# Optimization experiments

Measured on AMD Instinct MI355X. Metric: run time of the kernel, lower is better.

Reference implementation:

```python
import jax, jax.numpy as jnp
import numpy as np

N, E = 50000, 800000
H, KC, EC, NH = 64, 64, 32, 4   # hidden, key, edge channels, heads
HPH, KPH = H // NH, KC // NH    # per-head value/key dims (16, 16)


def ssp(x):
    # ShiftedSoftplus
    return jax.nn.softplus(x) - jnp.log(2.0).astype(x.dtype)


def grouped_lin(x, w):
    # x: (N, NH, in_per_head), w: (NH, out_per_head, in_per_head)
    # equivalent to Conv1d(kernel=1, groups=NH, bias=False)
    return jnp.einsum('nhi,hoi->nho', x, w)


def lin(x, w, b):
    return x @ w.T + b


def segment_softmax(logits, seg, num_segments):
    # logits: (E, NH), seg: (E,)
    m = jax.ops.segment_max(logits, seg, num_segments=num_segments)
    m = jnp.where(jnp.isfinite(m), m, 0.0)
    e = jnp.exp(logits - m[seg])
    s = jax.ops.segment_sum(e, seg, num_segments=num_segments)
    return e / s[seg]


def setup_inputs() -> dict:
    key = jax.random.key(0)
    ks = jax.random.split(key, 24)
    sc = 0.05
    inp = {
        'x': jax.random.normal(ks[0], (N, H), jnp.float32),
        'edge_index': jax.random.randint(ks[1], (2, E), 0, N, jnp.int64),
        'edge_attr': jax.random.normal(ks[2], (E, EC), jnp.float32),
        # grouped 1x1 convs (block-diagonal linears), no bias
        'k_w': jax.random.normal(ks[3], (NH, KPH, HPH), jnp.float32) * sc,
        'q_w': jax.random.normal(ks[4], (NH, KPH, HPH), jnp.float32) * sc,
        'v_w': jax.random.normal(ks[5], (NH, HPH, HPH), jnp.float32) * sc,
        # weight_k_net: Linear(EC,KPH) -> ssp -> Linear(KPH,KPH)
        'wkn_w1': jax.random.normal(ks[6], (KPH, EC), jnp.float32) * sc,
        'wkn_b1': jnp.zeros((KPH,), jnp.float32),
        'wkn_w2': jax.random.normal(ks[7], (KPH, KPH), jnp.float32) * sc,
        'wkn_b2': jnp.zeros((KPH,), jnp.float32),
        'wkl_w': jax.random.normal(ks[8], (KPH, KPH), jnp.float32) * sc,
        'wkl_b': jnp.zeros((KPH,), jnp.float32),
        # weight_v_net: Linear(EC,HPH) -> ssp -> Linear(HPH,HPH)
        'wvn_w1': jax.random.normal(ks[9], (HPH, EC), jnp.float32) * sc,
        'wvn_b1': jnp.zeros((HPH,), jnp.float32),
        'wvn_w2': jax.random.normal(ks[10], (HPH, HPH), jnp.float32) * sc,
        'wvn_b2': jnp.zeros((HPH,), jnp.float32),
        'wvl_w': jax.random.normal(ks[11], (HPH, HPH), jnp.float32) * sc,
        'wvl_b': jnp.zeros((HPH,), jnp.float32),
        'cen_w': jax.random.normal(ks[12], (H, H), jnp.float32) * sc,
        'cen_b': jnp.zeros((H,), jnp.float32),
        'out_w': jax.random.normal(ks[13], (H, H), jnp.float32) * sc,
        'out_b': jnp.zeros((H,), jnp.float32),
    }
    return inp


def reference(x, edge_index, edge_attr, k_w, q_w, v_w,
              wkn_w1, wkn_b1, wkn_w2, wkn_b2, wkl_w, wkl_b,
              wvn_w1, wvn_b1, wvn_w2, wvn_b2, wvl_w, wvl_b,
              cen_w, cen_b, out_w, out_b):
    n = x.shape[0]
    row, col = edge_index[0], edge_index[1]
    xh = x.reshape(n, NH, HPH)                       # per-head split of channels
    h_keys = grouped_lin(xh, k_w)                    # (N, NH, KPH)
    h_queries = grouped_lin(xh, q_w)                 # (N, NH, KPH)
    h_values = grouped_lin(xh, v_w)                  # (N, NH, HPH)

    W_k = lin(ssp(lin(edge_attr, wkn_w1, wkn_b1)), wkn_w2, wkn_b2)   # (E, KPH)
    keys_j = lin(W_k[:, None, :] * h_keys[col], wkl_w, wkl_b)        # (E, NH, KPH)
    queries_i = h_queries[row]                                       # (E, NH, KPH)
    qk_ij = jnp.sum(queries_i * keys_j, axis=-1)                     # (E, NH)
    alpha = segment_softmax(qk_ij, row, n)                           # (E, NH)

    W_v = lin(ssp(lin(edge_attr, wvn_w1, wvn_b1)), wvn_w2, wvn_b2)   # (E, HPH)
    msg_j = lin(W_v[:, None, :] * h_values[col], wvl_w, wvl_b)       # (E, NH, HPH)
    msg_j = alpha[:, :, None] * msg_j
    aggr = jax.ops.segment_sum(msg_j, row, num_segments=n).reshape(n, H)

    out = lin(x, cen_w, cen_b) + aggr
    return lin(ssp(out), out_w, out_b)
```

## Files before the change

kernel.cpp:

```cpp
#include <hip/hip_runtime.h>
#include <math.h>
#include <stdint.h>

#define NN 50000
#define NE 800000
#define HD 64
#define ECH 32
#define NHEAD 4
#define NBLK 196

static_assert(NE % 256 == 0, "edge kernel assumes full blocks");

typedef __attribute__((ext_vector_type(8))) short bf8;
typedef __attribute__((ext_vector_type(4))) float f32x4;

__device__ __forceinline__ float ssp_f(float v) {
    return fmaxf(v, 0.0f) + log1pf(__expf(-fabsf(v))) - 0.69314718055994531f;
}
__device__ __forceinline__ uint32_t f2bf_bits(float f) {
    uint32_t u = __float_as_uint(f);
    return (u + 0x7FFFu + ((u >> 16) & 1u)) >> 16;
}
__device__ __forceinline__ float bf2f(uint32_t b) { return __uint_as_float(b << 16); }

__device__ __forceinline__ void unpack8(uint4 p, float* o) {
    o[0] = bf2f(p.x & 0xffffu); o[1] = bf2f(p.x >> 16);
    o[2] = bf2f(p.y & 0xffffu); o[3] = bf2f(p.y >> 16);
    o[4] = bf2f(p.z & 0xffffu); o[5] = bf2f(p.z >> 16);
    o[6] = bf2f(p.w & 0xffffu); o[7] = bf2f(p.w >> 16);
}
__device__ __forceinline__ uint4 pack8u(const float* s) {
    uint4 r;
    r.x = f2bf_bits(s[0]) | (f2bf_bits(s[1]) << 16);
    r.y = f2bf_bits(s[2]) | (f2bf_bits(s[3]) << 16);
    r.z = f2bf_bits(s[4]) | (f2bf_bits(s[5]) << 16);
    r.w = f2bf_bits(s[6]) | (f2bf_bits(s[7]) << 16);
    return r;
}
__device__ __forceinline__ bf8 pack_bf8(float4 a, float4 b) {
    bf8 r;
    r[0] = (short)f2bf_bits(a.x); r[1] = (short)f2bf_bits(a.y);
    r[2] = (short)f2bf_bits(a.z); r[3] = (short)f2bf_bits(a.w);
    r[4] = (short)f2bf_bits(b.x); r[5] = (short)f2bf_bits(b.y);
    r[6] = (short)f2bf_bits(b.z); r[7] = (short)f2bf_bits(b.w);
    return r;
}
__device__ __forceinline__ bf8 zero_bf8() {
    bf8 r;
    #pragma unroll
    for (int i = 0; i < 8; ++i) r[i] = 0;
    return r;
}

__global__ __launch_bounds__(256) void node_transform_kernel(
    const float* __restrict__ x,
    const float* __restrict__ k_w, const float* __restrict__ q_w, const float* __restrict__ v_w,
    const float* __restrict__ wkl_w, const float* __restrict__ wkl_b,
    uint16_t* __restrict__ qt, float* __restrict__ qb,
    uint16_t* __restrict__ hk, uint16_t* __restrict__ hv)
{
    __shared__ float skw[NHEAD * 256], sqw[NHEAD * 256], svw[NHEAD * 256];
    __shared__ float s_kl[256], s_klb[16];
    for (int i = threadIdx.x; i < NHEAD * 256; i += 256) {
        skw[i] = k_w[i]; sqw[i] = q_w[i]; svw[i] = v_w[i];
    }
    if (threadIdx.x < 256) s_kl[threadIdx.x] = wkl_w[threadIdx.x];
    if (threadIdx.x < 16) s_klb[threadIdx.x] = wkl_b[threadIdx.x];
    __syncthreads();
    int n = blockIdx.x * 256 + threadIdx.x;
    if (n >= NN) return;
    const float* xn = x + (size_t)n * HD;
    float qbv[NHEAD];
    for (int h = 0; h < NHEAD; ++h) {
        float xr[16];
        {
            const float4* xp = (const float4*)(xn + h * 16);
            #pragma unroll
            for (int j = 0; j < 4; ++j) *(float4*)&xr[4 * j] = xp[j];
        }
        float rq[16], rk[16], rv[16];
        for (int o = 0; o < 16; ++o) {
            const float* wq = sqw + h * 256 + o * 16;
            const float* wk = skw + h * 256 + o * 16;
            const float* wv = svw + h * 256 + o * 16;
            float sq = 0.f, sk = 0.f, sv = 0.f;
            #pragma unroll
            for (int i = 0; i < 16; ++i) {
                sq += xr[i] * wq[i];
                sk += xr[i] * wk[i];
                sv += xr[i] * wv[i];
            }
            rq[o] = sq; rk[o] = sk; rv[o] = sv;
        }
        float rqt[16];
        float qbh = 0.f;
        for (int i = 0; i < 16; ++i) {
            float s = 0.f;
            #pragma unroll
            for (int o = 0; o < 16; ++o) s += rq[o] * s_kl[o * 16 + i];
            rqt[i] = s;
        }
        #pragma unroll
        for (int o = 0; o < 16; ++o) qbh += rq[o] * s_klb[o];
        qbv[h] = qbh;

        uint4* oq = (uint4*)(qt + (size_t)n * HD + h * 16);
        uint4* ok = (uint4*)(hk + (size_t)n * HD + h * 16);
        uint4* ov = (uint4*)(hv + (size_t)n * HD + h * 16);
        oq[0] = pack8u(rqt); oq[1] = pack8u(rqt + 8);
        ok[0] = pack8u(rk);  ok[1] = pack8u(rk + 8);
        ov[0] = pack8u(rv);  ov[1] = pack8u(rv + 8);
    }
    *(float4*)(qb + (size_t)n * NHEAD) = *(float4*)&qbv[0];
}

__global__ __launch_bounds__(256) void count_kernel(
    const int* __restrict__ ei, int* __restrict__ counts)
{
    int e = blockIdx.x * 256 + threadIdx.x;
    if (e >= NE) return;
    atomicAdd(counts + ei[e], 1);
}

__global__ __launch_bounds__(256) void scan_bsum_kernel(
    const int* __restrict__ counts, int* __restrict__ bsum)
{
    __shared__ int sd[256];
    int i = blockIdx.x * 256 + threadIdx.x;
    sd[threadIdx.x] = (i < NN) ? counts[i] : 0;
    __syncthreads();
    for (int s = 128; s > 0; s >>= 1) {
        if (threadIdx.x < (unsigned)s) sd[threadIdx.x] += sd[threadIdx.x + s];
        __syncthreads();
    }
    if (threadIdx.x == 0) bsum[blockIdx.x] = sd[0];
}

__global__ __launch_bounds__(256) void scan_top_kernel(int* __restrict__ bsum)
{
    __shared__ int tmp[256];
    int v = (threadIdx.x < NBLK) ? bsum[threadIdx.x] : 0;
    tmp[threadIdx.x] = v;
    __syncthreads();
    for (int d = 1; d < 256; d <<= 1) {
        int t = (threadIdx.x >= (unsigned)d) ? tmp[threadIdx.x - d] : 0;
        __syncthreads();
        tmp[threadIdx.x] += t;
        __syncthreads();
    }
    if (threadIdx.x < NBLK) bsum[threadIdx.x] = tmp[threadIdx.x] - v;
}

__global__ __launch_bounds__(256) void scan_final_kernel(
    const int* __restrict__ counts, const int* __restrict__ bsum,
    int* __restrict__ offsets, int* __restrict__ cursor)
{
    __shared__ int tmp[256];
    int i = blockIdx.x * 256 + threadIdx.x;
    int v = (i < NN) ? counts[i] : 0;
    tmp[threadIdx.x] = v;
    __syncthreads();
    for (int d = 1; d < 256; d <<= 1) {
        int t = (threadIdx.x >= (unsigned)d) ? tmp[threadIdx.x - d] : 0;
        __syncthreads();
        tmp[threadIdx.x] += t;
        __syncthreads();
    }
    int excl = tmp[threadIdx.x] - v + bsum[blockIdx.x];
    if (i < NN) { offsets[i] = excl; cursor[i] = excl; }
}

__global__ __launch_bounds__(256) void scatter_kernel(
    const int* __restrict__ ei, int* __restrict__ cursor,
    int* __restrict__ elist, int2* __restrict__ rc)
{
    int e = blockIdx.x * 256 + threadIdx.x;
    if (e >= NE) return;
    int r = ei[e];
    int c = ei[NE + e];
    int pos = atomicAdd(cursor + r, 1);
    elist[pos] = e;
    rc[pos] = make_int2(r, c);
}

__global__ __launch_bounds__(256) void edge_compute_kernel(
    const int* __restrict__ elist, const int2* __restrict__ rc,
    const float* __restrict__ ea,
    const float* __restrict__ wkn_w1, const float* __restrict__ wkn_b1,
    const float* __restrict__ wkn_w2, const float* __restrict__ wkn_b2,
    const float* __restrict__ wvn_w1, const float* __restrict__ wvn_b1,
    const float* __restrict__ wvn_w2, const float* __restrict__ wvn_b2,
    const uint16_t* __restrict__ qt, const float* __restrict__ qb,
    const uint16_t* __restrict__ hk, const uint16_t* __restrict__ hv,
    uint16_t* __restrict__ payload, float* __restrict__ wfac)
{
    __shared__ uint16_t s_tr1[4][64][24];
    __shared__ uint16_t s_trk[4][64][24];
    __shared__ uint16_t s_trv[4][64][24];

    const int w = threadIdx.x >> 6;
    const int L = threadIdx.x & 63;
    const int m = L & 15;
    const int g = L >> 4;
    const int ebase = blockIdx.x * 256 + w * 64;

    int2 rcv[4];
    #pragma unroll
    for (int t = 0; t < 4; ++t) rcv[t] = rc[ebase + 16 * t + m];

    bf8 eaf[4];
    #pragma unroll
    for (int t = 0; t < 4; ++t) {
        int eid = elist[ebase + 16 * t + m];
        const float* er = ea + (size_t)eid * ECH + 8 * g;
        eaf[t] = pack_bf8(*(const float4*)er, *(const float4*)(er + 4));
    }
    bf8 w1kf, w1vf, w2kf, w2vf;
    {
        const float* p = wkn_w1 + m * 32 + 8 * g;
        w1kf = pack_bf8(*(const float4*)p, *(const float4*)(p + 4));
        p = wvn_w1 + m * 32 + 8 * g;
        w1vf = pack_bf8(*(const float4*)p, *(const float4*)(p + 4));
        if (g < 2) {
            p = wkn_w2 + m * 16 + 8 * g;
            w2kf = pack_bf8(*(const float4*)p, *(const float4*)(p + 4));
            p = wvn_w2 + m * 16 + 8 * g;
            w2vf = pack_bf8(*(const float4*)p, *(const float4*)(p + 4));
        } else {
            w2kf = zero_bf8(); w2vf = zero_bf8();
        }
    }
    float4 b1k = *(const float4*)(wkn_b1 + 4 * g);
    float4 b1v = *(const float4*)(wvn_b1 + 4 * g);
    float4 b2k = *(const float4*)(wkn_b2 + 4 * g);
    float4 b2v = *(const float4*)(wvn_b2 + 4 * g);

    #pragma unroll
    for (int t = 0; t < 4; ++t) {
        f32x4 acc = {b1k.x, b1k.y, b1k.z, b1k.w};
        acc = __builtin_amdgcn_mfma_f32_16x16x32_bf16(w1kf, eaf[t], acc, 0, 0, 0);
        uint2 pk;
        pk.x = f2bf_bits(ssp_f(acc[0])) | (f2bf_bits(ssp_f(acc[1])) << 16);
        pk.y = f2bf_bits(ssp_f(acc[2])) | (f2bf_bits(ssp_f(acc[3])) << 16);
        *(uint2*)&s_tr1[w][16 * t + m][4 * g] = pk;
    }
    bf8 l1k[4];
    #pragma unroll
    for (int t = 0; t < 4; ++t)
        l1k[t] = (g < 2) ? *(const bf8*)&s_tr1[w][16 * t + m][8 * g] : zero_bf8();
    #pragma unroll
    for (int t = 0; t < 4; ++t) {
        f32x4 acc = {b1v.x, b1v.y, b1v.z, b1v.w};
        acc = __builtin_amdgcn_mfma_f32_16x16x32_bf16(w1vf, eaf[t], acc, 0, 0, 0);
        uint2 pk;
        pk.x = f2bf_bits(ssp_f(acc[0])) | (f2bf_bits(ssp_f(acc[1])) << 16);
        pk.y = f2bf_bits(ssp_f(acc[2])) | (f2bf_bits(ssp_f(acc[3])) << 16);
        *(uint2*)&s_tr1[w][16 * t + m][4 * g] = pk;
    }
    bf8 l1v[4];
    #pragma unroll
    for (int t = 0; t < 4; ++t)
        l1v[t] = (g < 2) ? *(const bf8*)&s_tr1[w][16 * t + m][8 * g] : zero_bf8();

    #pragma unroll
    for (int t = 0; t < 4; ++t) {
        f32x4 acc = {b2k.x, b2k.y, b2k.z, b2k.w};
        acc = __builtin_amdgcn_mfma_f32_16x16x32_bf16(w2kf, l1k[t], acc, 0, 0, 0);
        uint2 pk;
        pk.x = f2bf_bits(acc[0]) | (f2bf_bits(acc[1]) << 16);
        pk.y = f2bf_bits(acc[2]) | (f2bf_bits(acc[3]) << 16);
        *(uint2*)&s_trk[w][16 * t + m][4 * g] = pk;

        f32x4 accv = {b2v.x, b2v.y, b2v.z, b2v.w};
        accv = __builtin_amdgcn_mfma_f32_16x16x32_bf16(w2vf, l1v[t], accv, 0, 0, 0);
        uint2 pv;
        pv.x = f2bf_bits(accv[0]) | (f2bf_bits(accv[1]) << 16);
        pv.y = f2bf_bits(accv[2]) | (f2bf_bits(accv[3]) << 16);
        *(uint2*)&s_trv[w][16 * t + m][4 * g] = pv;
    }

    #pragma unroll
    for (int t = 0; t < 4; ++t) {
        const int E = ebase + 16 * t + m;
        const int row = rcv[t].x, col = rcv[t].y;

        float Wk[16], Wv[16];
        unpack8(*(const uint4*)&s_trk[w][16 * t + m][0], Wk);
        unpack8(*(const uint4*)&s_trk[w][16 * t + m][8], Wk + 8);
        unpack8(*(const uint4*)&s_trv[w][16 * t + m][0], Wv);
        unpack8(*(const uint4*)&s_trv[w][16 * t + m][8], Wv + 8);

        const uint4* qp = (const uint4*)(qt + (size_t)row * HD + 16 * g);
        const uint4* kp = (const uint4*)(hk + (size_t)col * HD + 16 * g);
        const uint4* vp = (const uint4*)(hv + (size_t)col * HD + 16 * g);
        float qr[16], kc[16], vc[16];
        unpack8(qp[0], qr); unpack8(qp[1], qr + 8);
        unpack8(kp[0], kc); unpack8(kp[1], kc + 8);
        unpack8(vp[0], vc); unpack8(vp[1], vc + 8);

        float qk = qb[(size_t)row * NHEAD + g];
        #pragma unroll
        for (int i = 0; i < 16; ++i) qk += qr[i] * Wk[i] * kc[i];
        float wgt = __expf(qk);

        float o[16];
        #pragma unroll
        for (int i = 0; i < 16; ++i) o[i] = wgt * Wv[i] * vc[i];
        uint4* pd = (uint4*)(payload + (size_t)E * HD + 16 * g);
        pd[0] = pack8u(o);
        pd[1] = pack8u(o + 8);
        wfac[(size_t)E * NHEAD + g] = wgt;
    }
}

__global__ __launch_bounds__(256) void gather_finalize_kernel(
    const float* __restrict__ x,
    const uint16_t* __restrict__ payload, const float* __restrict__ wfac,
    const int* __restrict__ offsets, const int* __restrict__ counts,
    const float* __restrict__ wvl_w, const float* __restrict__ wvl_b,
    const float* __restrict__ cen_w, const float* __restrict__ cen_b,
    const float* __restrict__ out_w, const float* __restrict__ out_b,
    float* __restrict__ out)
{
    __shared__ float s_cw[4096], s_ow[4096];
    __shared__ float s_wvl[256], s_vlb[16];
    __shared__ float s_m[4][64], s_x[4][64], s_t[4][64];
    for (int idx = threadIdx.x; idx < 4096; idx += 256) {
        int o = idx & 63, i = idx >> 6;
        s_cw[i * 64 + o] = cen_w[o * 64 + i];
        s_ow[i * 64 + o] = out_w[o * 64 + i];
    }
    if (threadIdx.x < 256) s_wvl[threadIdx.x] = wvl_w[threadIdx.x];
    if (threadIdx.x < 16) s_vlb[threadIdx.x] = wvl_b[threadIdx.x];
    __syncthreads();

    int l = threadIdx.x >> 6;
    int L = threadIdx.x & 63;
    int q = L & 7;
    int g = L >> 3;
    int h = q >> 1;

    for (int t = 0; t < 16; ++t) {
        int n = blockIdx.x * 64 + l * 16 + t;
        bool valid = n < NN;
        int st = 0, deg = 0;
        if (valid) { st = offsets[n]; deg = counts[n]; }
        float u[8] = {0.f, 0.f, 0.f, 0.f, 0.f, 0.f, 0.f, 0.f};
        float ds = 0.f;
        const uint16_t* pp = payload + (size_t)st * HD + 8 * q;
        const float* wp = wfac + (size_t)st * NHEAD + h;
        int iters = (deg + 7) >> 3;
        for (int i = 0; i < iters; ++i) {
            int e = 8 * i + g;
            if (e < deg) {
                uint4 pv = *(const uint4*)(pp + (size_t)e * HD);
                u[0] += bf2f(pv.x & 0xffffu); u[1] += bf2f(pv.x >> 16);
                u[2] += bf2f(pv.y & 0xffffu); u[3] += bf2f(pv.y >> 16);
                u[4] += bf2f(pv.z & 0xffffu); u[5] += bf2f(pv.z >> 16);
                u[6] += bf2f(pv.w & 0xffffu); u[7] += bf2f(pv.w >> 16);
                ds += wp[(size_t)e * NHEAD];
            }
        }
        #pragma unroll
        for (int s = 8; s < 64; s <<= 1) {
            #pragma unroll
            for (int j = 0; j < 8; ++j) u[j] += __shfl_xor(u[j], s);
            ds += __shfl_xor(ds, s);
        }
        if (g == 0) {
            float inv = (deg > 0) ? (1.f / ds) : 0.f;
            float r0[4] = {u[0] * inv, u[1] * inv, u[2] * inv, u[3] * inv};
            float r1[4] = {u[4] * inv, u[5] * inv, u[6] * inv, u[7] * inv};
            *(float4*)&s_m[l][8 * q] = *(float4*)r0;
            *(float4*)&s_m[l][8 * q + 4] = *(float4*)r1;
        }
        s_x[l][L] = valid ? x[(size_t)n * HD + L] : 0.f;

        int c = L, hh = c >> 4;
        float aggr = 0.f;
        if (deg > 0) {
            int o = c & 15;
            float s = s_vlb[o];
            #pragma unroll
            for (int i = 0; i < 16; ++i) s += s_m[l][hh * 16 + i] * s_wvl[o * 16 + i];
            aggr = s;
        }
        float sc = cen_b[c];
        #pragma unroll 8
        for (int i = 0; i < 64; ++i) sc += s_x[l][i] * s_cw[i * 64 + c];
        sc += aggr;
        s_t[l][c] = ssp_f(sc);
        float so = out_b[c];
        #pragma unroll 8
        for (int i = 0; i < 64; ++i) so += s_t[l][i] * s_ow[i * 64 + c];
        if (valid) out[(size_t)n * HD + c] = so;
    }
}

extern "C" void kernel_launch(void* const* d_in, const int* in_sizes, int n_in,
                              void* d_out, int out_size, void* d_ws, size_t ws_size,
                              hipStream_t stream)
{
    const float* x      = (const float*)d_in[0];
    const int*   ei     = (const int*)d_in[1];
    const float* ea     = (const float*)d_in[2];
    const float* k_w    = (const float*)d_in[3];
    const float* q_w    = (const float*)d_in[4];
    const float* v_w    = (const float*)d_in[5];
    const float* wkn_w1 = (const float*)d_in[6];
    const float* wkn_b1 = (const float*)d_in[7];
    const float* wkn_w2 = (const float*)d_in[8];
    const float* wkn_b2 = (const float*)d_in[9];
    const float* wkl_w  = (const float*)d_in[10];
    const float* wkl_b  = (const float*)d_in[11];
    const float* wvn_w1 = (const float*)d_in[12];
    const float* wvn_b1 = (const float*)d_in[13];
    const float* wvn_w2 = (const float*)d_in[14];
    const float* wvn_b2 = (const float*)d_in[15];
    const float* wvl_w  = (const float*)d_in[16];
    const float* wvl_b  = (const float*)d_in[17];
    const float* cen_w  = (const float*)d_in[18];
    const float* cen_b  = (const float*)d_in[19];
    const float* out_w  = (const float*)d_in[20];
    const float* out_b  = (const float*)d_in[21];
    float* out = (float*)d_out;

    float* qb    = (float*)d_ws;
    float* wfac  = qb + (size_t)NN * NHEAD;
    uint16_t* qt = (uint16_t*)(wfac + (size_t)NE * NHEAD);
    uint16_t* hk = qt + (size_t)NN * HD;
    uint16_t* hv = hk + (size_t)NN * HD;
    uint16_t* payload = hv + (size_t)NN * HD;
    int2* rc     = (int2*)(payload + (size_t)NE * HD);
    int* elist   = (int*)(rc + (size_t)NE);
    int* counts  = elist + NE;
    int* bsum    = counts + NN;
    int* offsets = bsum + 256;
    int* cursor  = offsets + NN;

    hipMemsetAsync(counts, 0, (size_t)NN * sizeof(int), stream);
    node_transform_kernel<<<NBLK, 256, 0, stream>>>(
        x, k_w, q_w, v_w, wkl_w, wkl_b, qt, qb, hk, hv);
    count_kernel<<<(NE + 255) / 256, 256, 0, stream>>>(ei, counts);
    scan_bsum_kernel<<<NBLK, 256, 0, stream>>>(counts, bsum);
    scan_top_kernel<<<1, 256, 0, stream>>>(bsum);
    scan_final_kernel<<<NBLK, 256, 0, stream>>>(counts, bsum, offsets, cursor);
    scatter_kernel<<<(NE + 255) / 256, 256, 0, stream>>>(ei, cursor, elist, rc);
    edge_compute_kernel<<<NE / 256, 256, 0, stream>>>(
        elist, rc, ea, wkn_w1, wkn_b1, wkn_w2, wkn_b2,
        wvn_w1, wvn_b1, wvn_w2, wvn_b2,
        qt, qb, hk, hv, payload, wfac);
    gather_finalize_kernel<<<(NN + 63) / 64, 256, 0, stream>>>(
        x, payload, wfac, offsets, counts,
        wvl_w, wvl_b, cen_w, cen_b, out_w, out_b, out);
}
```

Measured before the change: 516.7 us.

## Fuse per-edge aggregation into edge kernel via LDS atomics, drop payload buffer

The edge kernel now accumulates weighted messages and softmax denominators per destination row. It uses shared-memory atomics over a window of up to CAP rows, then flushes to global numer/denom, using atomics only at the block-boundary rows or when the window overflows. This replaces the bf16 per-edge payload and the separate gather pass. The scatter kernel also writes edge attributes pre-sorted and converted to bf16, so the edge kernel no longer does an indirect fp32 read. The cost is a larger memset, LDS atomic contention, float atomic nondeterminism, and the unnormalized exp with no max subtraction that the base code already used.

```diff
diff --git a/kernel.cpp b/kernel.cpp
--- a/kernel.cpp
+++ b/kernel.cpp
@@ -8,6 +8,7 @@
 #define ECH 32
 #define NHEAD 4
 #define NBLK 196
+#define CAP 80
 
 static_assert(NE % 256 == 0, "edge kernel assumes full blocks");
 
@@ -153,7 +154,7 @@
 
 __global__ __launch_bounds__(256) void scan_final_kernel(
     const int* __restrict__ counts, const int* __restrict__ bsum,
-    int* __restrict__ offsets, int* __restrict__ cursor)
+    int* __restrict__ cursor)
 {
     __shared__ int tmp[256];
     int i = blockIdx.x * 256 + threadIdx.x;
@@ -167,42 +168,60 @@
         __syncthreads();
     }
     int excl = tmp[threadIdx.x] - v + bsum[blockIdx.x];
-    if (i < NN) { offsets[i] = excl; cursor[i] = excl; }
+    if (i < NN) cursor[i] = excl;
 }
 
 __global__ __launch_bounds__(256) void scatter_kernel(
-    const int* __restrict__ ei, int* __restrict__ cursor,
-    int* __restrict__ elist, int2* __restrict__ rc)
+    const int* __restrict__ ei, const float* __restrict__ ea,
+    int* __restrict__ cursor,
+    int2* __restrict__ rc, uint16_t* __restrict__ eaS)
 {
     int e = blockIdx.x * 256 + threadIdx.x;
     if (e >= NE) return;
     int r = ei[e];
     int c = ei[NE + e];
+    float eav[32];
+    const float4* p = (const float4*)(ea + (size_t)e * ECH);
+    #pragma unroll
+    for (int i = 0; i < 8; ++i) *(float4*)&eav[4 * i] = p[i];
     int pos = atomicAdd(cursor + r, 1);
-    elist[pos] = e;
     rc[pos] = make_int2(r, c);
-}
-
-__global__ __launch_bounds__(256) void edge_compute_kernel(
-    const int* __restrict__ elist, const int2* __restrict__ rc,
-    const float* __restrict__ ea,
+    uint4* d = (uint4*)(eaS + (size_t)pos * ECH);
+    d[0] = pack8u(eav);      d[1] = pack8u(eav + 8);
+    d[2] = pack8u(eav + 16); d[3] = pack8u(eav + 24);
+}
+
+__global__ __launch_bounds__(256) void edge_fused_kernel(
+    const int2* __restrict__ rc, const uint16_t* __restrict__ eaS,
     const float* __restrict__ wkn_w1, const float* __restrict__ wkn_b1,
     const float* __restrict__ wkn_w2, const float* __restrict__ wkn_b2,
     const float* __restrict__ wvn_w1, const float* __restrict__ wvn_b1,
     const float* __restrict__ wvn_w2, const float* __restrict__ wvn_b2,
     const uint16_t* __restrict__ qt, const float* __restrict__ qb,
     const uint16_t* __restrict__ hk, const uint16_t* __restrict__ hv,
-    uint16_t* __restrict__ payload, float* __restrict__ wfac)
-{
-    __shared__ uint16_t s_tr1[4][64][24];
-    __shared__ uint16_t s_trk[4][64][24];
-    __shared__ uint16_t s_trv[4][64][24];
+    float* __restrict__ numer, float* __restrict__ denom)
+{
+    __shared__ uint16_t s_trA[4][64][24];
+    __shared__ uint16_t s_trB[4][64][24];
+    __shared__ float s_acc[CAP][68];
+
+    {
+        float4* az = (float4*)&s_acc[0][0];
+        float4 z = {0.f, 0.f, 0.f, 0.f};
+        for (int i = threadIdx.x; i < CAP * 68 / 4; i += 256) az[i] = z;
+    }
 
     const int w = threadIdx.x >> 6;
     const int L = threadIdx.x & 63;
     const int m = L & 15;
     const int g = L >> 4;
-    const int ebase = blockIdx.x * 256 + w * 64;
+    const int bbase = blockIdx.x * 256;
+    const int ebase = bbase + w * 64;
+
+    const int r0    = rc[bbase].x;
+    const int rlast = rc[bbase + 255].x;
+    const int nrows = rlast - r0 + 1;
+    const bool overflow = nrows > CAP;
 
     int2 rcv[4];
     #pragma unroll
@@ -210,11 +229,9 @@
 
     bf8 eaf[4];
     #pragma unroll
-    for (int t = 0; t < 4; ++t) {
-        int eid = elist[ebase + 16 * t + m];
-        const float* er = ea + (size_t)eid * ECH + 8 * g;
-        eaf[t] = pack_bf8(*(const float4*)er, *(const float4*)(er + 4));
-    }
+    for (int t = 0; t < 4; ++t)
+        eaf[t] = *(const bf8*)(eaS + (size_t)(ebase + 16 * t + m) * ECH + 8 * g);
+
     bf8 w1kf, w1vf, w2kf, w2vf;
     {
         const float* p = wkn_w1 + m * 32 + 8 * g;
@@ -242,12 +259,12 @@
         uint2 pk;
         pk.x = f2bf_bits(ssp_f(acc[0])) | (f2bf_bits(ssp_f(acc[1])) << 16);
         pk.y = f2bf_bits(ssp_f(acc[2])) | (f2bf_bits(ssp_f(acc[3])) << 16);
-        *(uint2*)&s_tr1[w][16 * t + m][4 * g] = pk;
+        *(uint2*)&s_trA[w][16 * t + m][4 * g] = pk;
     }
     bf8 l1k[4];
     #pragma unroll
     for (int t = 0; t < 4; ++t)
-        l1k[t] = (g < 2) ? *(const bf8*)&s_tr1[w][16 * t + m][8 * g] : zero_bf8();
+        l1k[t] = (g < 2) ? *(const bf8*)&s_trA[w][16 * t + m][8 * g] : zero_bf8();
     #pragma unroll
     for (int t = 0; t < 4; ++t) {
         f32x4 acc = {b1v.x, b1v.y, b1v.z, b1v.w};
@@ -255,12 +272,12 @@
         uint2 pk;
         pk.x = f2bf_bits(ssp_f(acc[0])) | (f2bf_bits(ssp_f(acc[1])) << 16);
         pk.y = f2bf_bits(ssp_f(acc[2])) | (f2bf_bits(ssp_f(acc[3])) << 16);
-        *(uint2*)&s_tr1[w][16 * t + m][4 * g] = pk;
+        *(uint2*)&s_trA[w][16 * t + m][4 * g] = pk;
     }
     bf8 l1v[4];
     #pragma unroll
     for (int t = 0; t < 4; ++t)
-        l1v[t] = (g < 2) ? *(const bf8*)&s_tr1[w][16 * t + m][8 * g] : zero_bf8();
+        l1v[t] = (g < 2) ? *(const bf8*)&s_trA[w][16 * t + m][8 * g] : zero_bf8();
 
     #pragma unroll
     for (int t = 0; t < 4; ++t) {
@@ -269,26 +286,27 @@
         uint2 pk;
         pk.x = f2bf_bits(acc[0]) | (f2bf_bits(acc[1]) << 16);
         pk.y = f2bf_bits(acc[2]) | (f2bf_bits(acc[3]) << 16);
-        *(uint2*)&s_trk[w][16 * t + m][4 * g] = pk;
+        *(uint2*)&s_trB[w][16 * t + m][4 * g] = pk;
 
         f32x4 accv = {b2v.x, b2v.y, b2v.z, b2v.w};
         accv = __builtin_amdgcn_mfma_f32_16x16x32_bf16(w2vf, l1v[t], accv, 0, 0, 0);
         uint2 pv;
         pv.x = f2bf_bits(accv[0]) | (f2bf_bits(accv[1]) << 16);
         pv.y = f2bf_bits(accv[2]) | (f2bf_bits(accv[3]) << 16);
-        *(uint2*)&s_trv[w][16 * t + m][4 * g] = pv;
-    }
+        *(uint2*)&s_trA[w][16 * t + m][4 * g] = pv;
+    }
+
+    __syncthreads();
 
     #pragma unroll
     for (int t = 0; t < 4; ++t) {
-        const int E = ebase + 16 * t + m;
         const int row = rcv[t].x, col = rcv[t].y;
 
         float Wk[16], Wv[16];
-        unpack8(*(const uint4*)&s_trk[w][16 * t + m][0], Wk);
-        unpack8(*(const uint4*)&s_trk[w][16 * t + m][8], Wk + 8);
-        unpack8(*(const uint4*)&s_trv[w][16 * t + m][0], Wv);
-        unpack8(*(const uint4*)&s_trv[w][16 * t + m][8], Wv + 8);
+        unpack8(*(const uint4*)&s_trB[w][16 * t + m][0], Wk);
+        unpack8(*(const uint4*)&s_trB[w][16 * t + m][8], Wk + 8);
+        unpack8(*(const uint4*)&s_trA[w][16 * t + m][0], Wv);
+        unpack8(*(const uint4*)&s_trA[w][16 * t + m][8], Wv + 8);
 
         const uint4* qp = (const uint4*)(qt + (size_t)row * HD + 16 * g);
         const uint4* kp = (const uint4*)(hk + (size_t)col * HD + 16 * g);
@@ -303,20 +321,37 @@
         for (int i = 0; i < 16; ++i) qk += qr[i] * Wk[i] * kc[i];
         float wgt = __expf(qk);
 
-        float o[16];
-        #pragma unroll
-        for (int i = 0; i < 16; ++i) o[i] = wgt * Wv[i] * vc[i];
-        uint4* pd = (uint4*)(payload + (size_t)E * HD + 16 * g);
-        pd[0] = pack8u(o);
-        pd[1] = pack8u(o + 8);
-        wfac[(size_t)E * NHEAD + g] = wgt;
-    }
-}
-
-__global__ __launch_bounds__(256) void gather_finalize_kernel(
+        int idx = row - r0;
+        if (idx < CAP) {
+            float* ar = &s_acc[idx][16 * g];
+            #pragma unroll
+            for (int i = 0; i < 16; ++i) atomicAdd(ar + i, wgt * Wv[i] * vc[i]);
+            atomicAdd(&s_acc[idx][64 + g], wgt);
+        } else {
+            float* nr = numer + (size_t)row * HD + 16 * g;
+            #pragma unroll
+            for (int i = 0; i < 16; ++i) atomicAdd(nr + i, wgt * Wv[i] * vc[i]);
+            atomicAdd(denom + (size_t)row * NHEAD + g, wgt);
+        }
+    }
+    __syncthreads();
+
+    const int lim = (nrows < CAP) ? nrows : CAP;
+    for (int j = threadIdx.x; j < lim * 68; j += 256) {
+        int ridx = j / 68;
+        int c = j - ridx * 68;
+        float v = s_acc[ridx][c];
+        bool at = overflow || (ridx == 0) || (ridx == lim - 1);
+        float* dst = (c < 64) ? (numer + (size_t)(r0 + ridx) * HD + c)
+                              : (denom + (size_t)(r0 + ridx) * NHEAD + (c - 64));
+        if (at) atomicAdd(dst, v);
+        else    *dst = v;
+    }
+}
+
+__global__ __launch_bounds__(256) void finalize_kernel(
     const float* __restrict__ x,
-    const uint16_t* __restrict__ payload, const float* __restrict__ wfac,
-    const int* __restrict__ offsets, const int* __restrict__ counts,
+    const float* __restrict__ numer, const float* __restrict__ denom,
     const float* __restrict__ wvl_w, const float* __restrict__ wvl_b,
     const float* __restrict__ cen_w, const float* __restrict__ cen_b,
     const float* __restrict__ out_w, const float* __restrict__ out_b,
@@ -336,64 +371,34 @@
 
     int l = threadIdx.x >> 6;
     int L = threadIdx.x & 63;
-    int q = L & 7;
-    int g = L >> 3;
-    int h = q >> 1;
+    int h = L >> 4;
 
     for (int t = 0; t < 16; ++t) {
         int n = blockIdx.x * 64 + l * 16 + t;
         bool valid = n < NN;
-        int st = 0, deg = 0;
-        if (valid) { st = offsets[n]; deg = counts[n]; }
-        float u[8] = {0.f, 0.f, 0.f, 0.f, 0.f, 0.f, 0.f, 0.f};
-        float ds = 0.f;
-        const uint16_t* pp = payload + (size_t)st * HD + 8 * q;
-        const float* wp = wfac + (size_t)st * NHEAD + h;
-        int iters = (deg + 7) >> 3;
-        for (int i = 0; i < iters; ++i) {
-            int e = 8 * i + g;
-            if (e < deg) {
-                uint4 pv = *(const uint4*)(pp + (size_t)e * HD);
-                u[0] += bf2f(pv.x & 0xffffu); u[1] += bf2f(pv.x >> 16);
-                u[2] += bf2f(pv.y & 0xffffu); u[3] += bf2f(pv.y >> 16);
-                u[4] += bf2f(pv.z & 0xffffu); u[5] += bf2f(pv.z >> 16);
-                u[6] += bf2f(pv.w & 0xffffu); u[7] += bf2f(pv.w >> 16);
-                ds += wp[(size_t)e * NHEAD];
-            }
-        }
-        #pragma unroll
-        for (int s = 8; s < 64; s <<= 1) {
-            #pragma unroll
-            for (int j = 0; j < 8; ++j) u[j] += __shfl_xor(u[j], s);
-            ds += __shfl_xor(ds, s);
-        }
-        if (g == 0) {
-            float inv = (deg > 0) ? (1.f / ds) : 0.f;
-            float r0[4] = {u[0] * inv, u[1] * inv, u[2] * inv, u[3] * inv};
-            float r1[4] = {u[4] * inv, u[5] * inv, u[6] * inv, u[7] * inv};
-            *(float4*)&s_m[l][8 * q] = *(float4*)r0;
-            *(float4*)&s_m[l][8 * q + 4] = *(float4*)r1;
-        }
+        float d = valid ? denom[(size_t)n * NHEAD + h] : 0.f;
+        float num = valid ? numer[(size_t)n * HD + L] : 0.f;
+        bool has = d != 0.f;
+        s_m[l][L] = has ? num / d : 0.f;
         s_x[l][L] = valid ? x[(size_t)n * HD + L] : 0.f;
 
-        int c = L, hh = c >> 4;
         float aggr = 0.f;
-        if (deg > 0) {
-            int o = c & 15;
+        if (has) {
+            int o = L & 15;
             float s = s_vlb[o];
             #pragma unroll
-            for (int i = 0; i < 16; ++i) s += s_m[l][hh * 16 + i] * s_wvl[o * 16 + i];
+            for (int i = 0; i < 16; ++i) s += s_m[l][h * 16 + i] * s_wvl[o * 16 + i];
             aggr = s;
         }
-        float sc = cen_b[c];
+        float sc = cen_b[L];
         #pragma unroll 8
-        for (int i = 0; i < 64; ++i) sc += s_x[l][i] * s_cw[i * 64 + c];
+        for (int i = 0; i < 64; ++i) sc += s_x[l][i] * s_cw[i * 64 + L];
         sc += aggr;
-        s_t[l][c] = ssp_f(sc);
-        float so = out_b[c];
+        s_t[l][L] = ssp_f(sc);
+        float so = out_b[L];
         #pragma unroll 8
-        for (int i = 0; i < 64; ++i) so += s_t[l][i] * s_ow[i * 64 + c];
-        if (valid) out[(size_t)n * HD + c] = so;
+        for (int i = 0; i < 64; ++i) so += s_t[l][i] * s_ow[i * 64 + L];
+        if (valid) out[(size_t)n * HD + L] = so;
     }
 }
 
@@ -425,32 +430,31 @@
     const float* out_b  = (const float*)d_in[21];
     float* out = (float*)d_out;
 
-    float* qb    = (float*)d_ws;
-    float* wfac  = qb + (size_t)NN * NHEAD;
-    uint16_t* qt = (uint16_t*)(wfac + (size_t)NE * NHEAD);
+    float* numer = (float*)d_ws;
+    float* denom = numer + (size_t)NN * HD;
+    int* counts  = (int*)(denom + (size_t)NN * NHEAD);
+    int* bsum    = counts + NN;
+    int* cursor  = bsum + 256;
+    float* qb    = (float*)(cursor + NN);
+    uint16_t* qt = (uint16_t*)(qb + (size_t)NN * NHEAD);
     uint16_t* hk = qt + (size_t)NN * HD;
     uint16_t* hv = hk + (size_t)NN * HD;
-    uint16_t* payload = hv + (size_t)NN * HD;
-    int2* rc     = (int2*)(payload + (size_t)NE * HD);
-    int* elist   = (int*)(rc + (size_t)NE);
-    int* counts  = elist + NE;
-    int* bsum    = counts + NN;
-    int* offsets = bsum + 256;
-    int* cursor  = offsets + NN;
-
-    hipMemsetAsync(counts, 0, (size_t)NN * sizeof(int), stream);
+    int2* rc     = (int2*)(hv + (size_t)NN * HD);
+    uint16_t* eaS = (uint16_t*)(rc + (size_t)NE);
+
+    size_t zero_bytes = (size_t)NN * HD * 4 + (size_t)NN * NHEAD * 4 + (size_t)NN * 4;
+    hipMemsetAsync(numer, 0, zero_bytes, stream);
     node_transform_kernel<<<NBLK, 256, 0, stream>>>(
         x, k_w, q_w, v_w, wkl_w, wkl_b, qt, qb, hk, hv);
     count_kernel<<<(NE + 255) / 256, 256, 0, stream>>>(ei, counts);
     scan_bsum_kernel<<<NBLK, 256, 0, stream>>>(counts, bsum);
     scan_top_kernel<<<1, 256, 0, stream>>>(bsum);
-    scan_final_kernel<<<NBLK, 256, 0, stream>>>(counts, bsum, offsets, cursor);
-    scatter_kernel<<<(NE + 255) / 256, 256, 0, stream>>>(ei, cursor, elist, rc);
-    edge_compute_kernel<<<NE / 256, 256, 0, stream>>>(
-        elist, rc, ea, wkn_w1, wkn_b1, wkn_w2, wkn_b2,
+    scan_final_kernel<<<NBLK, 256, 0, stream>>>(counts, bsum, cursor);
+    scatter_kernel<<<(NE + 255) / 256, 256, 0, stream>>>(ei, ea, cursor, rc, eaS);
+    edge_fused_kernel<<<NE / 256, 256, 0, stream>>>(
+        rc, eaS, wkn_w1, wkn_b1, wkn_w2, wkn_b2,
         wvn_w1, wvn_b1, wvn_w2, wvn_b2,
-        qt, qb, hk, hv, payload, wfac);
-    gather_finalize_kernel<<<(NN + 63) / 64, 256, 0, stream>>>(
-        x, payload, wfac, offsets, counts,
-        wvl_w, wvl_b, cen_w, cen_b, out_w, out_b, out);
-}
+        qt, qb, hk, hv, numer, denom);
+    finalize_kernel<<<(NN + 63) / 64, 256, 0, stream>>>(
+        x, numer, denom, wvl_w, wvl_b, cen_w, cen_b, out_w, out_b, out);
+}
```

Result: slower. 824.0 us (+59.5%).

## Fuse count into node transform, interleave node tables, shuffle-broadcast offsets

Applied to the files above, without the earlier changes.

Merges the edge-degree counting kernel into the node transform kernel, removing one launch; the first 196 blocks also do node work. Node outputs are repacked so q and its bias share a 72-element row and keys and values share a 128-element row, so each gathered edge touches fewer cache lines. The edge kernel drops one shared-memory transpose buffer, and the gather kernel loads offsets and counts once per wave and broadcasts them with shuffles. The risks are load imbalance in the fused kernel and 144-byte q rows that are not aligned to cache lines.

```diff
diff --git a/kernel.cpp b/kernel.cpp
--- a/kernel.cpp
+++ b/kernel.cpp
@@ -8,6 +8,7 @@
 #define ECH 32
 #define NHEAD 4
 #define NBLK 196
+#define NEBLK (NE / 256)
 
 static_assert(NE % 256 == 0, "edge kernel assumes full blocks");
 
@@ -52,13 +53,16 @@
     return r;
 }
 
-__global__ __launch_bounds__(256) void node_transform_kernel(
-    const float* __restrict__ x,
+__global__ __launch_bounds__(256) void node_count_kernel(
+    const float* __restrict__ x, const int* __restrict__ ei,
     const float* __restrict__ k_w, const float* __restrict__ q_w, const float* __restrict__ v_w,
     const float* __restrict__ wkl_w, const float* __restrict__ wkl_b,
-    uint16_t* __restrict__ qt, float* __restrict__ qb,
-    uint16_t* __restrict__ hk, uint16_t* __restrict__ hv)
-{
+    uint16_t* __restrict__ qtq, uint16_t* __restrict__ hkv,
+    int* __restrict__ counts)
+{
+    atomicAdd(counts + ei[blockIdx.x * 256 + threadIdx.x], 1);
+
+    if (blockIdx.x >= NBLK) return;
     __shared__ float skw[NHEAD * 256], sqw[NHEAD * 256], svw[NHEAD * 256];
     __shared__ float s_kl[256], s_klb[16];
     for (int i = threadIdx.x; i < NHEAD * 256; i += 256) {
@@ -70,6 +74,8 @@
     int n = blockIdx.x * 256 + threadIdx.x;
     if (n >= NN) return;
     const float* xn = x + (size_t)n * HD;
+    uint16_t* qrow = qtq + (size_t)n * 72;
+    uint16_t* kvrow = hkv + (size_t)n * 128;
     float qbv[NHEAD];
     for (int h = 0; h < NHEAD; ++h) {
         float xr[16];
@@ -104,22 +110,14 @@
         for (int o = 0; o < 16; ++o) qbh += rq[o] * s_klb[o];
         qbv[h] = qbh;
 
-        uint4* oq = (uint4*)(qt + (size_t)n * HD + h * 16);
-        uint4* ok = (uint4*)(hk + (size_t)n * HD + h * 16);
-        uint4* ov = (uint4*)(hv + (size_t)n * HD + h * 16);
+        uint4* oq = (uint4*)(qrow + h * 16);
+        uint4* ok = (uint4*)(kvrow + h * 16);
+        uint4* ov = (uint4*)(kvrow + 64 + h * 16);
         oq[0] = pack8u(rqt); oq[1] = pack8u(rqt + 8);
         ok[0] = pack8u(rk);  ok[1] = pack8u(rk + 8);
         ov[0] = pack8u(rv);  ov[1] = pack8u(rv + 8);
     }
-    *(float4*)(qb + (size_t)n * NHEAD) = *(float4*)&qbv[0];
-}
-
-__global__ __launch_bounds__(256) void count_kernel(
-    const int* __restrict__ ei, int* __restrict__ counts)
-{
-    int e = blockIdx.x * 256 + threadIdx.x;
-    if (e >= NE) return;
-    atomicAdd(counts + ei[e], 1);
+    *(float4*)(qrow + 64) = *(float4*)&qbv[0];
 }
 
 __global__ __launch_bounds__(256) void scan_bsum_kernel(
@@ -190,13 +188,11 @@
     const float* __restrict__ wkn_w2, const float* __restrict__ wkn_b2,
     const float* __restrict__ wvn_w1, const float* __restrict__ wvn_b1,
     const float* __restrict__ wvn_w2, const float* __restrict__ wvn_b2,
-    const uint16_t* __restrict__ qt, const float* __restrict__ qb,
-    const uint16_t* __restrict__ hk, const uint16_t* __restrict__ hv,
+    const uint16_t* __restrict__ qtq, const uint16_t* __restrict__ hkv,
     uint16_t* __restrict__ payload, float* __restrict__ wfac)
 {
-    __shared__ uint16_t s_tr1[4][64][24];
-    __shared__ uint16_t s_trk[4][64][24];
-    __shared__ uint16_t s_trv[4][64][24];
+    __shared__ uint16_t s_trA[4][64][24];
+    __shared__ uint16_t s_trB[4][64][24];
 
     const int w = threadIdx.x >> 6;
     const int L = threadIdx.x & 63;
@@ -204,15 +200,17 @@
     const int g = L >> 4;
     const int ebase = blockIdx.x * 256 + w * 64;
 
+    int eidv[4];
     int2 rcv[4];
     #pragma unroll
+    for (int t = 0; t < 4; ++t) eidv[t] = elist[ebase + 16 * t + m];
+    #pragma unroll
     for (int t = 0; t < 4; ++t) rcv[t] = rc[ebase + 16 * t + m];
 
     bf8 eaf[4];
     #pragma unroll
     for (int t = 0; t < 4; ++t) {
-        int eid = elist[ebase + 16 * t + m];
-        const float* er = ea + (size_t)eid * ECH + 8 * g;
+        const float* er = ea + (size_t)eidv[t] * ECH + 8 * g;
         eaf[t] = pack_bf8(*(const float4*)er, *(const float4*)(er + 4));
     }
     bf8 w1kf, w1vf, w2kf, w2vf;
@@ -242,12 +240,12 @@
         uint2 pk;
         pk.x = f2bf_bits(ssp_f(acc[0])) | (f2bf_bits(ssp_f(acc[1])) << 16);
         pk.y = f2bf_bits(ssp_f(acc[2])) | (f2bf_bits(ssp_f(acc[3])) << 16);
-        *(uint2*)&s_tr1[w][16 * t + m][4 * g] = pk;
+        *(uint2*)&s_trA[w][16 * t + m][4 * g] = pk;
     }
     bf8 l1k[4];
     #pragma unroll
     for (int t = 0; t < 4; ++t)
-        l1k[t] = (g < 2) ? *(const bf8*)&s_tr1[w][16 * t + m][8 * g] : zero_bf8();
+        l1k[t] = (g < 2) ? *(const bf8*)&s_trA[w][16 * t + m][8 * g] : zero_bf8();
     #pragma unroll
     for (int t = 0; t < 4; ++t) {
         f32x4 acc = {b1v.x, b1v.y, b1v.z, b1v.w};
@@ -255,12 +253,12 @@
         uint2 pk;
         pk.x = f2bf_bits(ssp_f(acc[0])) | (f2bf_bits(ssp_f(acc[1])) << 16);
         pk.y = f2bf_bits(ssp_f(acc[2])) | (f2bf_bits(ssp_f(acc[3])) << 16);
-        *(uint2*)&s_tr1[w][16 * t + m][4 * g] = pk;
+        *(uint2*)&s_trA[w][16 * t + m][4 * g] = pk;
     }
     bf8 l1v[4];
     #pragma unroll
     for (int t = 0; t < 4; ++t)
-        l1v[t] = (g < 2) ? *(const bf8*)&s_tr1[w][16 * t + m][8 * g] : zero_bf8();
+        l1v[t] = (g < 2) ? *(const bf8*)&s_trA[w][16 * t + m][8 * g] : zero_bf8();
 
     #pragma unroll
     for (int t = 0; t < 4; ++t) {
@@ -269,14 +267,14 @@
         uint2 pk;
         pk.x = f2bf_bits(acc[0]) | (f2bf_bits(acc[1]) << 16);
         pk.y = f2bf_bits(acc[2]) | (f2bf_bits(acc[3]) << 16);
-        *(uint2*)&s_trk[w][16 * t + m][4 * g] = pk;
+        *(uint2*)&s_trB[w][16 * t + m][4 * g] = pk;
 
         f32x4 accv = {b2v.x, b2v.y, b2v.z, b2v.w};
         accv = __builtin_amdgcn_mfma_f32_16x16x32_bf16(w2vf, l1v[t], accv, 0, 0, 0);
         uint2 pv;
         pv.x = f2bf_bits(accv[0]) | (f2bf_bits(accv[1]) << 16);
         pv.y = f2bf_bits(accv[2]) | (f2bf_bits(accv[3]) << 16);
-        *(uint2*)&s_trv[w][16 * t + m][4 * g] = pv;
+        *(uint2*)&s_trA[w][16 * t + m][4 * g] = pv;
     }
 
     #pragma unroll
@@ -285,20 +283,22 @@
         const int row = rcv[t].x, col = rcv[t].y;
 
         float Wk[16], Wv[16];
-        unpack8(*(const uint4*)&s_trk[w][16 * t + m][0], Wk);
-        unpack8(*(const uint4*)&s_trk[w][16 * t + m][8], Wk + 8);
-        unpack8(*(const uint4*)&s_trv[w][16 * t + m][0], Wv);
-        unpack8(*(const uint4*)&s_trv[w][16 * t + m][8], Wv + 8);
-
-        const uint4* qp = (const uint4*)(qt + (size_t)row * HD + 16 * g);
-        const uint4* kp = (const uint4*)(hk + (size_t)col * HD + 16 * g);
-        const uint4* vp = (const uint4*)(hv + (size_t)col * HD + 16 * g);
+        unpack8(*(const uint4*)&s_trB[w][16 * t + m][0], Wk);
+        unpack8(*(const uint4*)&s_trB[w][16 * t + m][8], Wk + 8);
+        unpack8(*(const uint4*)&s_trA[w][16 * t + m][0], Wv);
+        unpack8(*(const uint4*)&s_trA[w][16 * t + m][8], Wv + 8);
+
+        const uint16_t* qrow = qtq + (size_t)row * 72;
+        const uint16_t* kvrow = hkv + (size_t)col * 128;
+        const uint4* qp = (const uint4*)(qrow + 16 * g);
+        const uint4* kp = (const uint4*)(kvrow + 16 * g);
+        const uint4* vp = (const uint4*)(kvrow + 64 + 16 * g);
         float qr[16], kc[16], vc[16];
         unpack8(qp[0], qr); unpack8(qp[1], qr + 8);
         unpack8(kp[0], kc); unpack8(kp[1], kc + 8);
         unpack8(vp[0], vc); unpack8(vp[1], vc + 8);
 
-        float qk = qb[(size_t)row * NHEAD + g];
+        float qk = *(const float*)(qrow + 64 + 2 * g);
         #pragma unroll
         for (int i = 0; i < 16; ++i) qk += qr[i] * Wk[i] * kc[i];
         float wgt = __expf(qk);
@@ -340,11 +340,18 @@
     int g = L >> 3;
     int h = q >> 1;
 
+    int n0 = blockIdx.x * 64 + l * 16;
+    int pj = n0 + (L & 15);
+    bool pvalid = pj < NN;
+    int offv = 0, cntv = 0;
+    if (L < 16) offv = pvalid ? offsets[pj] : 0;
+    else if (L < 32) cntv = pvalid ? counts[pj] : 0;
+
     for (int t = 0; t < 16; ++t) {
-        int n = blockIdx.x * 64 + l * 16 + t;
+        int n = n0 + t;
         bool valid = n < NN;
-        int st = 0, deg = 0;
-        if (valid) { st = offsets[n]; deg = counts[n]; }
+        int st = __shfl(offv, t);
+        int deg = valid ? __shfl(cntv, 16 + t) : 0;
         float u[8] = {0.f, 0.f, 0.f, 0.f, 0.f, 0.f, 0.f, 0.f};
         float ds = 0.f;
         const uint16_t* pp = payload + (size_t)st * HD + 8 * q;
@@ -425,12 +432,10 @@
     const float* out_b  = (const float*)d_in[21];
     float* out = (float*)d_out;
 
-    float* qb    = (float*)d_ws;
-    float* wfac  = qb + (size_t)NN * NHEAD;
-    uint16_t* qt = (uint16_t*)(wfac + (size_t)NE * NHEAD);
-    uint16_t* hk = qt + (size_t)NN * HD;
-    uint16_t* hv = hk + (size_t)NN * HD;
-    uint16_t* payload = hv + (size_t)NN * HD;
+    float* wfac  = (float*)d_ws;
+    uint16_t* qtq = (uint16_t*)(wfac + (size_t)NE * NHEAD);
+    uint16_t* hkv = qtq + (size_t)NN * 72;
+    uint16_t* payload = hkv + (size_t)NN * 128;
     int2* rc     = (int2*)(payload + (size_t)NE * HD);
     int* elist   = (int*)(rc + (size_t)NE);
     int* counts  = elist + NE;
@@ -439,17 +444,16 @@
     int* cursor  = offsets + NN;
 
     hipMemsetAsync(counts, 0, (size_t)NN * sizeof(int), stream);
-    node_transform_kernel<<<NBLK, 256, 0, stream>>>(
-        x, k_w, q_w, v_w, wkl_w, wkl_b, qt, qb, hk, hv);
-    count_kernel<<<(NE + 255) / 256, 256, 0, stream>>>(ei, counts);
+    node_count_kernel<<<NEBLK, 256, 0, stream>>>(
+        x, ei, k_w, q_w, v_w, wkl_w, wkl_b, qtq, hkv, counts);
     scan_bsum_kernel<<<NBLK, 256, 0, stream>>>(counts, bsum);
     scan_top_kernel<<<1, 256, 0, stream>>>(bsum);
     scan_final_kernel<<<NBLK, 256, 0, stream>>>(counts, bsum, offsets, cursor);
-    scatter_kernel<<<(NE + 255) / 256, 256, 0, stream>>>(ei, cursor, elist, rc);
-    edge_compute_kernel<<<NE / 256, 256, 0, stream>>>(
+    scatter_kernel<<<NEBLK, 256, 0, stream>>>(ei, cursor, elist, rc);
+    edge_compute_kernel<<<NEBLK, 256, 0, stream>>>(
         elist, rc, ea, wkn_w1, wkn_b1, wkn_w2, wkn_b2,
         wvn_w1, wvn_b1, wvn_w2, wvn_b2,
-        qt, qb, hk, hv, payload, wfac);
+        qtq, hkv, payload, wfac);
     gather_finalize_kernel<<<(NN + 63) / 64, 256, 0, stream>>>(
         x, payload, wfac, offsets, counts,
         wvl_w, wvl_b, cen_w, cen_b, out_w, out_b, out);
```

Result: faster. 498.3 us (-3.6%).
